# Kernel optimization log

Hardware: AMD Instinct MI355X
Metric: run time of the kernel (lower is better)

## Reference

```python
import jax, jax.numpy as jnp
import numpy as np

B, S, D = 4, 4096, 2048
H, HD = 16, 128
FFN = 8192
CAP = 0.25
TOP_K = int(S * CAP)  # 1024
EPS = 1e-6


def rmsnorm(x, g):
    return x * jax.lax.rsqrt(jnp.mean(x * x, axis=-1, keepdims=True) + EPS) * g


def apply_rope(x, cos, sin):
    # x: [b,t,h,hd]; cos/sin: [t, hd//2]
    half = x.shape[-1] // 2
    x1, x2 = x[..., :half], x[..., half:]
    c = cos[None, :, None, :]
    s = sin[None, :, None, :]
    return jnp.concatenate([x1 * c - x2 * s, x1 * s + x2 * c], axis=-1)


def transformer_block(x, mask, freqs_cis, g1, wq, wk, wv, wo, g2, w1, w3, w2):
    b, t, d = x.shape
    cos, sin = freqs_cis[..., 0], freqs_cis[..., 1]
    h = rmsnorm(x, g1)
    q = (h @ wq).reshape(b, t, H, HD)
    k = (h @ wk).reshape(b, t, H, HD)
    v = (h @ wv).reshape(b, t, H, HD)
    q = apply_rope(q, cos, sin)
    k = apply_rope(k, cos, sin)
    scores = jnp.einsum('bqhd,bkhd->bhqk', q, k) / np.sqrt(HD) + mask[None, None]
    attn = jax.nn.softmax(scores, axis=-1)
    o = jnp.einsum('bhqk,bkhd->bqhd', attn, v).reshape(b, t, d) @ wo
    x = x + o
    h2 = rmsnorm(x, g2)
    x = x + (jax.nn.silu(h2 @ w1) * (h2 @ w3)) @ w2
    return x, None


def setup_inputs() -> dict:
    key = jax.random.key(0)
    ks = jax.random.split(key, 12)
    w = lambda k, shp: jax.random.normal(k, shp, dtype=jnp.float32) * 0.02
    return {
        'x': jax.random.normal(ks[0], (B, S, D), dtype=jnp.float32),
        'mask': jnp.zeros((TOP_K, TOP_K), dtype=jnp.float32),
        'freqs_cis': jax.random.uniform(ks[1], (TOP_K, HD // 2, 2), dtype=jnp.float32),
        'w_router': w(ks[2], (D,)),
        'g1': jnp.ones((D,), dtype=jnp.float32),
        'wq': w(ks[3], (D, D)),
        'wk': w(ks[4], (D, D)),
        'wv': w(ks[5], (D, D)),
        'wo': w(ks[6], (D, D)),
        'g2': jnp.ones((D,), dtype=jnp.float32),
        'w1': w(ks[7], (D, FFN)),
        'w3': w(ks[8], (D, FFN)),
        'w2': w(ks[9], (FFN, D)),
    }


def reference(x, mask, freqs_cis, w_router, g1, wq, wk, wv, wo, g2, w1, w3, w2):
    b, s, d = x.shape
    # router: Linear(dim, 1, bias=False) -> [b, s]
    router_logits = jnp.einsum('bsd,d->bs', x, w_router)
    vals, idx = jax.lax.top_k(router_logits, TOP_K)  # [b, k]
    # sort selected indices ascending; permute weights to match (softmax is
    # permutation-equivariant so softmax-then-permute == torch's gather order)
    order = jnp.argsort(idx, axis=1)
    sel = jnp.take_along_axis(idx, order, axis=1)          # [b, k]
    w_sel = jnp.take_along_axis(vals, order, axis=1)       # [b, k]
    r_weights = jax.nn.softmax(w_sel, axis=1)[..., None]   # [b, k, 1]
    filtered_x = jnp.take_along_axis(x, sel[..., None], axis=1)  # [b, k, d]
    x_out, _ = transformer_block(filtered_x, mask, freqs_cis, g1, wq, wk, wv, wo, g2, w1, w3, w2)
    xw_out = r_weights * x_out
    b_idx = jnp.arange(b)[:, None]
    out = x.at[b_idx, sel].add(xw_out)
    return out
```

## Files before the change

kernel.cpp:

```cpp
#include <hip/hip_runtime.h>
#include <cstdint>
#include <cstddef>

#define NB 4
#define NS 4096
#define ND 2048
#define NH 16
#define NHD 128
#define NT 1024
#define NF 8192

typedef __bf16 bf16;
typedef __bf16 bf16x8 __attribute__((ext_vector_type(8)));
typedef __bf16 bf16x4 __attribute__((ext_vector_type(4)));
typedef float  f32x4  __attribute__((ext_vector_type(4)));

typedef const __attribute__((address_space(1))) void* gptr_t;
typedef __attribute__((address_space(3))) void* lptr_t;

__device__ __forceinline__ float wave_sum(float v) {
#pragma unroll
    for (int off = 32; off > 0; off >>= 1) v += __shfl_xor(v, off);
    return v;
}
__device__ __forceinline__ float wave_max(float v) {
#pragma unroll
    for (int off = 32; off > 0; off >>= 1) v = fmaxf(v, __shfl_xor(v, off));
    return v;
}

__global__ __launch_bounds__(256) void router_k(const float* __restrict__ x,
                                                const float* __restrict__ wr,
                                                float* __restrict__ logits) {
    __shared__ float r4[4];
    long long row = blockIdx.x;
    const float4* xr = (const float4*)(x + row * ND);
    const float4* w4 = (const float4*)wr;
    float p = 0.f;
    for (int i = threadIdx.x; i < ND / 4; i += 256) {
        float4 a = xr[i], b = w4[i];
        p += a.x * b.x + a.y * b.y + a.z * b.z + a.w * b.w;
    }
    p = wave_sum(p);
    if ((threadIdx.x & 63) == 0) r4[threadIdx.x >> 6] = p;
    __syncthreads();
    if (threadIdx.x == 0) logits[row] = r4[0] + r4[1] + r4[2] + r4[3];
}

__global__ __launch_bounds__(1024) void topk_k(const float* __restrict__ logits,
                                               int* __restrict__ sel,
                                               float* __restrict__ rw) {
    __shared__ unsigned long long keys[NS];
    __shared__ float r16[16];
    __shared__ float bmax, bsum;
    const int bb = blockIdx.x;
    const int tid = threadIdx.x;
    const float* lg = logits + (long long)bb * NS;

    for (int i = tid; i < NS; i += 1024) {
        unsigned u = __float_as_uint(lg[i]);
        u = (u & 0x80000000u) ? ~u : (u | 0x80000000u);
        keys[i] = ((unsigned long long)u << 32) | (unsigned)(NS - 1 - i);
    }
    __syncthreads();
    for (int k = 2; k <= NS; k <<= 1) {
        for (int j = k >> 1; j > 0; j >>= 1) {
            for (int i = tid; i < NS; i += 1024) {
                int ixj = i ^ j;
                if (ixj > i) {
                    unsigned long long a = keys[i], c = keys[ixj];
                    bool up = ((i & k) == 0);
                    if (up ? (a < c) : (a > c)) { keys[i] = c; keys[ixj] = a; }
                }
            }
            __syncthreads();
        }
    }
    unsigned long long a0 = keys[tid];
    __syncthreads();
    {
        unsigned idx_ = NS - 1 - (unsigned)(a0 & 0xFFFFFFFFu);
        unsigned uval = (unsigned)(a0 >> 32);
        keys[tid] = ((unsigned long long)idx_ << 32) | uval;
    }
    __syncthreads();
    for (int k = 2; k <= NT; k <<= 1) {
        for (int j = k >> 1; j > 0; j >>= 1) {
            int i = tid, ixj = i ^ j;
            if (i < NT && ixj > i) {
                unsigned long long a = keys[i], c = keys[ixj];
                bool up = ((i & k) == 0);
                if (up ? (a > c) : (a < c)) { keys[i] = c; keys[ixj] = a; }
            }
            __syncthreads();
        }
    }
    unsigned long long kk = keys[tid];
    int si = (int)(kk >> 32);
    unsigned u = (unsigned)(kk & 0xFFFFFFFFu);
    u = (u & 0x80000000u) ? (u ^ 0x80000000u) : ~u;
    float val = __uint_as_float(u);

    const int wid = tid >> 6, lane = tid & 63;
    float mx = wave_max(val);
    if (lane == 0) r16[wid] = mx;
    __syncthreads();
    if (tid == 0) {
        float m = r16[0];
        for (int i = 1; i < 16; i++) m = fmaxf(m, r16[i]);
        bmax = m;
    }
    __syncthreads();
    float e = __expf(val - bmax);
    float s = wave_sum(e);
    if (lane == 0) r16[wid] = s;
    __syncthreads();
    if (tid == 0) {
        float t = 0.f;
        for (int i = 0; i < 16; i++) t += r16[i];
        bsum = t;
    }
    __syncthreads();
    sel[bb * NT + tid] = si;
    rw[bb * NT + tid] = e / bsum;
}

__global__ __launch_bounds__(256) void gather_k(const float* __restrict__ x,
                                                const int* __restrict__ sel,
                                                float* __restrict__ xf) {
    int gid = blockIdx.x * 256 + threadIdx.x;
    int col = gid & (ND / 4 - 1);
    int row = gid >> 9;
    int bb = row >> 10;
    int s = sel[row];
    ((float4*)xf)[gid] = ((const float4*)x)[((long long)bb * NS + s) * (ND / 4) + col];
}

__global__ __launch_bounds__(256) void rmsnorm_k(const float* __restrict__ x,
                                                 const float* __restrict__ g,
                                                 bf16* __restrict__ out) {
    __shared__ float r4[4];
    __shared__ float scl;
    long long row = blockIdx.x;
    const float4* xr = (const float4*)(x + row * ND);
    int i0 = threadIdx.x, i1 = threadIdx.x + 256;
    float4 a = xr[i0], b = xr[i1];
    float ss = a.x * a.x + a.y * a.y + a.z * a.z + a.w * a.w +
               b.x * b.x + b.y * b.y + b.z * b.z + b.w * b.w;
    ss = wave_sum(ss);
    if ((threadIdx.x & 63) == 0) r4[threadIdx.x >> 6] = ss;
    __syncthreads();
    if (threadIdx.x == 0)
        scl = rsqrtf((r4[0] + r4[1] + r4[2] + r4[3]) * (1.0f / ND) + 1e-6f);
    __syncthreads();
    float s = scl;
    const float4* g4 = (const float4*)g;
    float4 ga = g4[i0], gb = g4[i1];
    bf16x4 o0, o1;
    o0[0] = (bf16)(a.x * s * ga.x); o0[1] = (bf16)(a.y * s * ga.y);
    o0[2] = (bf16)(a.z * s * ga.z); o0[3] = (bf16)(a.w * s * ga.w);
    o1[0] = (bf16)(b.x * s * gb.x); o1[1] = (bf16)(b.y * s * gb.y);
    o1[2] = (bf16)(b.z * s * gb.z); o1[3] = (bf16)(b.w * s * gb.w);
    *(bf16x4*)(out + row * ND + i0 * 4) = o0;
    *(bf16x4*)(out + row * ND + i1 * 4) = o1;
}

__global__ __launch_bounds__(256) void transpose_to_bf16(const float* __restrict__ in,
                                                         bf16* __restrict__ out,
                                                         int R, int C) {
    __shared__ float tile[32][33];
    int bx = blockIdx.x * 32;
    int by = blockIdx.y * 32;
    int tx = threadIdx.x & 31;
    int ty = threadIdx.x >> 5;
#pragma unroll
    for (int i = 0; i < 4; i++)
        tile[ty + 8 * i][tx] = in[(long long)(by + ty + 8 * i) * C + bx + tx];
    __syncthreads();
#pragma unroll
    for (int i = 0; i < 4; i++)
        out[(long long)(bx + ty + 8 * i) * R + by + tx] = (bf16)tile[tx][ty + 8 * i];
}

__global__ __launch_bounds__(256) void rope_qk_k(const bf16* __restrict__ QKV,
                                                 const float* __restrict__ fr,
                                                 bf16* __restrict__ Q,
                                                 bf16* __restrict__ K) {
    int gid = blockIdx.x * 256 + threadIdx.x;
    int hd = gid & 63;
    int h = (gid >> 6) & 15;
    int t = (gid >> 10) & (NT - 1);
    int bb = gid >> 20;
    float c = fr[t * 128 + hd * 2 + 0];
    float s = fr[t * 128 + hd * 2 + 1];
    long long base = ((long long)bb * NT + t) * (3 * ND) + h * NHD;
    float q1 = (float)QKV[base + hd],      q2 = (float)QKV[base + hd + 64];
    float k1 = (float)QKV[base + ND + hd], k2 = (float)QKV[base + ND + hd + 64];
    long long ob = (((long long)(bb * NH + h)) * NT + t) * NHD;
    Q[ob + hd]      = (bf16)(q1 * c - q2 * s);
    Q[ob + hd + 64] = (bf16)(q1 * s + q2 * c);
    K[ob + hd]      = (bf16)(k1 * c - k2 * s);
    K[ob + hd + 64] = (bf16)(k1 * s + k2 * c);
}

__global__ __launch_bounds__(256) void vtr_k(const bf16* __restrict__ QKV,
                                             bf16* __restrict__ Vt) {
    __shared__ bf16 tile[64][136];
    const int tt = blockIdx.x * 64;
    const int bh = blockIdx.y;
    const int bb = bh >> 4, h = bh & 15;
    const int tid = threadIdx.x;

    const int lt = tid >> 4;
    const int ld = (tid & 15) * 8;
#pragma unroll
    for (int i = 0; i < 4; i++) {
        int t = i * 16 + lt;
        bf16x8 v = *(const bf16x8*)(QKV + ((size_t)(bb * NT) + tt + t) * (3 * ND)
                                    + 2 * ND + h * NHD + ld);
        *(bf16x8*)&tile[t][ld] = v;
    }
    __syncthreads();

    const int d = tid >> 1;
    const int j0 = (tid & 1) * 32;
    bf16 tmp[32];
#pragma unroll
    for (int j = 0; j < 32; j++) tmp[j] = tile[j0 + j][d];
    bf16* dst = Vt + ((size_t)bh * NHD + d) * NT + tt + j0;
#pragma unroll
    for (int j = 0; j < 4; j++)
        *(bf16x8*)(dst + j * 8) = *(const bf16x8*)(tmp + j * 8);
}

__global__ __launch_bounds__(256) void copy_k(const float4* __restrict__ in,
                                              float4* __restrict__ out, long long n) {
    for (long long i = (long long)blockIdx.x * 256 + threadIdx.x; i < n;
         i += (long long)gridDim.x * 256)
        out[i] = in[i];
}

__global__ __launch_bounds__(256, 2) void flash_k(
    const bf16* __restrict__ Qr,
    const bf16* __restrict__ Kr,
    const bf16* __restrict__ Vt,
    bf16* __restrict__ O) {
    __shared__ char lds[81920];

    const int tid = threadIdx.x;
    const int lane = tid & 63;
    const int w = tid >> 6;
    const int lm = lane & 15, lq = lane >> 4;
    const int lm7 = lm & 7;

    const int bh = blockIdx.y;
    const int q0 = blockIdx.x * 128;
    const bf16* Qb = Qr + (size_t)bh * NT * NHD;
    const bf16* Kb = Kr + (size_t)bh * NT * NHD;
    const bf16* Vb = Vt + (size_t)bh * NHD * NT;

    const int krow = tid >> 4;
    const int kc_s = (tid & 15);
    const int vrow = tid >> 3;
    const int vc_s = (tid & 7);

    bf16x8 q[2][4];
#pragma unroll
    for (int mi = 0; mi < 2; mi++)
#pragma unroll
        for (int ks = 0; ks < 4; ks++)
            q[mi][ks] = *(const bf16x8*)(Qb + (size_t)(q0 + w * 32 + mi * 16 + lm) * NHD
                                         + lq * 8 + ks * 32);

    f32x4 o0[8], o1[8];
#pragma unroll
    for (int i = 0; i < 8; i++) {
        f32x4 zz = {0.f, 0.f, 0.f, 0.f};
        o0[i] = zz; o1[i] = zz;
    }
    float m0[4], m1[4], l0[4], l1[4];
#pragma unroll
    for (int r = 0; r < 4; r++) {
        m0[r] = -3.0e38f; m1[r] = -3.0e38f; l0[r] = 0.f; l1[r] = 0.f;
    }

    char* Pb = lds + 65536 + w * 4096;
    const float kscal = 0.08838834764831845f * 1.4426950408889634f;

#pragma unroll
    for (int i = 0; i < 4; i++) {
        int row = i * 16 + krow;
        __builtin_amdgcn_global_load_lds(
            (gptr_t)(Kb + (size_t)row * NHD + (kc_s ^ (row & 7)) * 8),
            (lptr_t)(lds + i * 4096 + tid * 16), 16, 0, 0);
    }
#pragma unroll
    for (int i = 0; i < 4; i++) {
        int row = i * 32 + vrow;
        __builtin_amdgcn_global_load_lds(
            (gptr_t)(Vb + (size_t)row * NT + (vc_s ^ (row & 7)) * 8),
            (lptr_t)(lds + 32768 + i * 4096 + tid * 16), 16, 0, 0);
    }
    __syncthreads();

    for (int c = 0; c < 16; ++c) {
        char* Kl = lds + (c & 1) * 16384;
        char* Vl = lds + 32768 + (c & 1) * 16384;

        if (c < 15) {
            const int key1 = (c + 1) * 64;
            char* Kd = lds + ((c + 1) & 1) * 16384;
            char* Vd = lds + 32768 + ((c + 1) & 1) * 16384;
#pragma unroll
            for (int i = 0; i < 4; i++) {
                int row = i * 16 + krow;
                __builtin_amdgcn_global_load_lds(
                    (gptr_t)(Kb + (size_t)(key1 + row) * NHD + (kc_s ^ (row & 7)) * 8),
                    (lptr_t)(Kd + i * 4096 + tid * 16), 16, 0, 0);
            }
#pragma unroll
            for (int i = 0; i < 4; i++) {
                int row = i * 32 + vrow;
                __builtin_amdgcn_global_load_lds(
                    (gptr_t)(Vb + (size_t)row * NT + key1 + (vc_s ^ (row & 7)) * 8),
                    (lptr_t)(Vd + i * 4096 + tid * 16), 16, 0, 0);
            }
        }

        f32x4 s0[4], s1[4];
#pragma unroll
        for (int ni = 0; ni < 4; ni++) {
            f32x4 zz = {0.f, 0.f, 0.f, 0.f};
            s0[ni] = zz; s1[ni] = zz;
        }
        __builtin_amdgcn_s_setprio(1);
#pragma unroll
        for (int ni = 0; ni < 4; ni++) {
#pragma unroll
            for (int ks = 0; ks < 4; ks++) {
                bf16x8 kf = *(const bf16x8*)(Kl + (lm + 16 * ni) * 256
                                             + (((lq + 4 * ks) ^ lm7) << 4));
                s0[ni] = __builtin_amdgcn_mfma_f32_16x16x32_bf16(q[0][ks], kf, s0[ni], 0, 0, 0);
                s1[ni] = __builtin_amdgcn_mfma_f32_16x16x32_bf16(q[1][ks], kf, s1[ni], 0, 0, 0);
            }
        }
        __builtin_amdgcn_s_setprio(0);

#pragma unroll
        for (int ni = 0; ni < 4; ni++)
#pragma unroll
            for (int r = 0; r < 4; r++) {
                s0[ni][r] *= kscal;
                s1[ni][r] *= kscal;
            }

        float sc0[4], sc1[4];
#pragma unroll
        for (int r = 0; r < 4; r++) {
            float a0 = fmaxf(fmaxf(s0[0][r], s0[1][r]), fmaxf(s0[2][r], s0[3][r]));
            float a1 = fmaxf(fmaxf(s1[0][r], s1[1][r]), fmaxf(s1[2][r], s1[3][r]));
#pragma unroll
            for (int o = 1; o < 16; o <<= 1) {
                a0 = fmaxf(a0, __shfl_xor(a0, o));
                a1 = fmaxf(a1, __shfl_xor(a1, o));
            }
            float mn0 = fmaxf(m0[r], a0);
            float mn1 = fmaxf(m1[r], a1);
            sc0[r] = exp2f(m0[r] - mn0);
            sc1[r] = exp2f(m1[r] - mn1);
            m0[r] = mn0; m1[r] = mn1;

            float rs0 = 0.f, rs1 = 0.f;
#pragma unroll
            for (int ni = 0; ni < 4; ni++) {
                float p0 = exp2f(s0[ni][r] - mn0);
                float p1 = exp2f(s1[ni][r] - mn1);
                s0[ni][r] = p0; s1[ni][r] = p1;
                rs0 += p0; rs1 += p1;
            }
#pragma unroll
            for (int o = 1; o < 16; o <<= 1) {
                rs0 += __shfl_xor(rs0, o);
                rs1 += __shfl_xor(rs1, o);
            }
            l0[r] = l0[r] * sc0[r] + rs0;
            l1[r] = l1[r] * sc1[r] + rs1;
        }
#pragma unroll
        for (int ni = 0; ni < 8; ni++)
#pragma unroll
            for (int r = 0; r < 4; r++) {
                o0[ni][r] *= sc0[r];
                o1[ni][r] *= sc1[r];
            }

#pragma unroll
        for (int ni = 0; ni < 4; ni++)
#pragma unroll
            for (int r = 0; r < 4; r++) {
                int q_l0 = lq * 4 + r;
                int q_l1 = 16 + q_l0;
                int cw = (lm >> 3) + 2 * ni;
                *(bf16*)(Pb + q_l0 * 128 + ((cw ^ (q_l0 & 7)) << 4) + (lm7 << 1)) =
                    (bf16)s0[ni][r];
                *(bf16*)(Pb + q_l1 * 128 + ((cw ^ (q_l1 & 7)) << 4) + (lm7 << 1)) =
                    (bf16)s1[ni][r];
            }
        asm volatile("s_waitcnt lgkmcnt(0)" ::: "memory");
        __builtin_amdgcn_sched_barrier(0);

        __builtin_amdgcn_s_setprio(1);
#pragma unroll
        for (int ks = 0; ks < 2; ks++) {
            bf16x8 pa0 = *(const bf16x8*)(Pb + lm * 128 + (((lq + 4 * ks) ^ lm7) << 4));
            bf16x8 pa1 = *(const bf16x8*)(Pb + (lm + 16) * 128 + (((lq + 4 * ks) ^ lm7) << 4));
#pragma unroll
            for (int ni = 0; ni < 8; ni++) {
                bf16x8 vf = *(const bf16x8*)(Vl + (lm + 16 * ni) * 128
                                             + (((lq + 4 * ks) ^ lm7) << 4));
                o0[ni] = __builtin_amdgcn_mfma_f32_16x16x32_bf16(pa0, vf, o0[ni], 0, 0, 0);
                o1[ni] = __builtin_amdgcn_mfma_f32_16x16x32_bf16(pa1, vf, o1[ni], 0, 0, 0);
            }
        }
        __builtin_amdgcn_s_setprio(0);

        __syncthreads();
    }

    const int bb = bh >> 4, h = bh & 15;
    float rl0[4], rl1[4];
#pragma unroll
    for (int r = 0; r < 4; r++) { rl0[r] = 1.f / l0[r]; rl1[r] = 1.f / l1[r]; }
#pragma unroll
    for (int ni = 0; ni < 8; ni++) {
#pragma unroll
        for (int r = 0; r < 4; r++) {
            int col = h * 128 + lm + 16 * ni;
            long long r0 = (long long)bb * NT + q0 + w * 32 + lq * 4 + r;
            O[(r0) * ND + col]      = (bf16)(o0[ni][r] * rl0[r]);
            O[(r0 + 16) * ND + col] = (bf16)(o1[ni][r] * rl1[r]);
        }
    }
}

#define G256_SB() __builtin_amdgcn_sched_barrier(0)
#define G256_LGKM(n) do { asm volatile("s_waitcnt lgkmcnt(" #n ")" ::: "memory"); \
    __builtin_amdgcn_sched_barrier(0); } while (0)
#define G256_VMC(n) do { asm volatile("s_waitcnt vmcnt(" #n ")" ::: "memory"); \
    __builtin_amdgcn_sched_barrier(0); } while (0)

#define MFMA_Q(mlo, nlo) do { \
    __builtin_amdgcn_s_setprio(1); \
    _Pragma("unroll") \
    for (int _ks = 0; _ks < 2; _ks++) \
    _Pragma("unroll") \
    for (int _mi = 0; _mi < 4; _mi++) \
    _Pragma("unroll") \
    for (int _ni = 0; _ni < 2; _ni++) \
        acc[(mlo) + _mi][(nlo) + _ni] = __builtin_amdgcn_mfma_f32_16x16x32_bf16( \
            a[(mlo) + _mi][_ks], b[(nlo) + _ni][_ks], acc[(mlo) + _mi][(nlo) + _ni], \
            0, 0, 0); \
    __builtin_amdgcn_s_setprio(0); \
} while (0)

template <int MODE>
__global__ __launch_bounds__(512, 2) void gemm256(
    const bf16* __restrict__ A, int lda,
    const bf16* __restrict__ Bt, int ldb,
    void* __restrict__ Cv, int ldc,
    int K, float alpha,
    const bf16* __restrict__ Bt2,
    const float* __restrict__ res, const int* __restrict__ selp,
    const float* __restrict__ rwp, float* __restrict__ outp) {

    constexpr bool DUALB = (MODE == 6);
    constexpr bool N128  = (MODE == 2 || MODE == 5);
    constexpr bool NI4   = !N128;
    constexpr int  BBUF  = N128 ? 16384 : 32768;
    constexpr int  BUFS  = 32768 + BBUF;
    constexpr int  bw    = (DUALB || N128) ? 32 : 64;
    constexpr int  bStep2 = DUALB ? 16384 : 4096;
    constexpr int  NIE   = (DUALB || N128) ? 2 : 4;
    __shared__ char smem[2 * BUFS];

    const int tid = threadIdx.x;
    const int lane = tid & 63;
    const int wid = tid >> 6;
    const int wm = wid >> 2, wn = wid & 3;
    const int lm = lane & 15, lq = lane >> 4;

    const int nx = gridDim.x;
    const int orig = blockIdx.y * nx + blockIdx.x;
    const int xcd = orig & 7;
    const int r_ = orig >> 3;
    const int mi_ = r_ & 7, ni_ = r_ >> 3;
    const int nT = (DUALB || N128) ? 128 : 256;
    const int m0 = ((xcd >> 2) * 8 + mi_) * 256;
    const int n0 = ((xcd & 3) * (nx >> 2) + ni_) * nT;
    const long long kz = (long long)blockIdx.z * K;

    const int srow = tid >> 3;
    const int skc = ((tid & 7) ^ (srow & 7)) * 8;
    const long long stA = (long long)64 * lda;
    const long long stB = (long long)64 * ldb;
    const bf16* gA = A + (long long)(m0 + srow) * lda + kz + skc;
    const bf16* gB0 = Bt + (long long)(n0 + srow) * ldb + kz + skc;
    const bf16* gB2 = DUALB ? Bt2 + (long long)(n0 + srow) * ldb + kz + skc
                            : gB0 + 2 * stB;

    char* sm = (char*)smem;
    const int sdst = tid * 16;

    auto stage = [&](int c, int t) {
        char* lA = sm + c * BUFS + sdst;
        long long ko = (long long)t * 64;
#pragma unroll
        for (int i = 0; i < 4; i++)
            __builtin_amdgcn_global_load_lds((gptr_t)(gA + i * stA + ko),
                                             (lptr_t)(lA + i * 8192), 16, 0, 0);
        char* lB = sm + c * BUFS + 32768 + sdst;
        __builtin_amdgcn_global_load_lds((gptr_t)(gB0 + ko), (lptr_t)lB, 16, 0, 0);
        __builtin_amdgcn_global_load_lds((gptr_t)(gB0 + stB + ko),
                                         (lptr_t)(lB + 8192), 16, 0, 0);
        if constexpr (NI4) {
            __builtin_amdgcn_global_load_lds((gptr_t)(gB2 + ko),
                                             (lptr_t)(lB + 16384), 16, 0, 0);
            __builtin_amdgcn_global_load_lds((gptr_t)(gB2 + stB + ko),
                                             (lptr_t)(lB + 24576), 16, 0, 0);
        }
    };

    const int aoff = (wm * 128 + lm) * 128 + ((lq ^ (lm & 7)) << 4);
    const int boff = (wn * bw + lm) * 128 + ((lq ^ (lm & 7)) << 4);

    f32x4 acc[8][4];
#pragma unroll
    for (int i = 0; i < 8; i++)
#pragma unroll
        for (int j = 0; j < 4; j++) {
            f32x4 zz = {0.f, 0.f, 0.f, 0.f};
            acc[i][j] = zz;
        }
    bf16x8 a[8][2], b[4][2];

    auto ldA4 = [&](char* bA, int lo) {
#pragma unroll
        for (int mi2 = 0; mi2 < 4; mi2++) {
            a[lo + mi2][0] = *(const bf16x8*)(bA + aoff + (lo + mi2) * 2048);
            a[lo + mi2][1] = *(const bf16x8*)(bA + (aoff ^ 64) + (lo + mi2) * 2048);
        }
    };
    auto ldB2 = [&](char* bB, int lo) {
#pragma unroll
        for (int ni2 = 0; ni2 < 2; ni2++) {
            int ix = lo + ni2;
            int o = boff + (ix & 1) * 2048 + (ix >> 1) * bStep2;
            b[ix][0] = *(const bf16x8*)(bB + o);
            b[ix][1] = *(const bf16x8*)(bB + (o ^ 64));
        }
    };

    const int NTk = K >> 6;

    stage(0, 0);
    stage(1, 1);
    if constexpr (NI4) { G256_VMC(8); } else { G256_VMC(6); }
    __builtin_amdgcn_s_barrier();
    G256_SB();

    for (int t = 0; t < NTk; ++t) {
        const int c = t & 1;
        char* bA = sm + c * BUFS;
        char* bB = bA + 32768;

        ldA4(bA, 0);
        ldB2(bB, 0);
        G256_SB();
        if constexpr (NI4) {
            ldB2(bB, 2);
            G256_SB();
        }
        ldA4(bA, 4);
        G256_SB();

        if constexpr (NI4) { G256_LGKM(12); } else { G256_LGKM(8); }
        MFMA_Q(0, 0);
        if constexpr (NI4) {
            G256_LGKM(8);
            MFMA_Q(0, 2);
        }
        G256_LGKM(0);
        __builtin_amdgcn_s_barrier();
        G256_SB();
        const bool more = (t + 2 < NTk);
        if (more) stage(c, t + 2);
        G256_SB();
        MFMA_Q(4, 0);
        if constexpr (NI4) MFMA_Q(4, 2);
        if (more) {
            if constexpr (NI4) { G256_VMC(8); } else { G256_VMC(6); }
        } else {
            G256_VMC(0);
        }
        __builtin_amdgcn_s_barrier();
        G256_SB();
    }

    if constexpr (MODE == 6) {
        bf16* C = (bf16*)Cv;
#pragma unroll
        for (int mi = 0; mi < 8; mi++) {
#pragma unroll
            for (int ni = 0; ni < 2; ni++) {
                const int row = m0 + wm * 128 + mi * 16 + lq * 4;
                const int col = n0 + wn * 32 + ni * 16 + lm;
#pragma unroll
                for (int r = 0; r < 4; r++) {
                    float v1 = acc[mi][ni][r];
                    float v3 = acc[mi][ni + 2][r];
                    C[(long long)(row + r) * ldc + col] =
                        (bf16)((v1 / (1.f + __expf(-v1))) * v3);
                }
            }
        }
    } else {
#pragma unroll
        for (int mi = 0; mi < 8; mi++) {
#pragma unroll
            for (int ni = 0; ni < NIE; ni++) {
                const int row = m0 + wm * 128 + mi * 16 + lq * 4;
                const int col = n0 + wn * bw + ni * 16 + lm;
#pragma unroll
                for (int r = 0; r < 4; r++) {
                    float v = alpha * acc[mi][ni][r];
                    long long rr = row + r;
                    if constexpr (MODE == 0) {
                        bf16* C = (bf16*)Cv;
                        C[rr * ldc + col] = (bf16)v;
                    } else if constexpr (MODE == 2) {
                        float* C = (float*)Cv;
                        C[rr * ldc + col] += v;
                    } else {
                        int bb2 = (int)(rr >> 10);
                        int s = selp[rr];
                        float add = rwp[rr] * (v + res[rr * (long long)ND + col]);
                        outp[((long long)bb2 * NS + s) * ND + col] += add;
                    }
                }
            }
        }
    }
}

extern "C" void kernel_launch(void* const* d_in, const int* in_sizes, int n_in,
                              void* d_out, int out_size, void* d_ws, size_t ws_size,
                              hipStream_t stream) {
    const float* x  = (const float*)d_in[0];
    const float* fr = (const float*)d_in[2];
    const float* wr = (const float*)d_in[3];
    const float* g1 = (const float*)d_in[4];
    const float* wq = (const float*)d_in[5];
    const float* wk = (const float*)d_in[6];
    const float* wv = (const float*)d_in[7];
    const float* wo = (const float*)d_in[8];
    const float* g2 = (const float*)d_in[9];
    const float* w1 = (const float*)d_in[10];
    const float* w3 = (const float*)d_in[11];
    const float* w2 = (const float*)d_in[12];
    float* out = (float*)d_out;

    char* ws = (char*)d_ws;
    size_t off = 0;
    auto take = [&](size_t bytes) -> char* {
        char* p = ws + off;
        off += (bytes + 255) & ~(size_t)255;
        return p;
    };
    int*   sel    = (int*)take((size_t)NB * NT * 4);
    float* rw     = (float*)take((size_t)NB * NT * 4);
    float* logits = (float*)take((size_t)NB * NS * 4);
    float* xf     = (float*)take((size_t)NB * NT * ND * 4);
    bf16*  hbuf   = (bf16*)take((size_t)NB * NT * ND * 2);
    bf16*  wqkv_t = (bf16*)take((size_t)3 * ND * ND * 2);
    bf16*  wo_t   = (bf16*)take((size_t)ND * ND * 2);
    bf16*  Obuf   = (bf16*)take((size_t)NB * NT * ND * 2);
    char* xr = ws + off;
    bf16* QKV = (bf16*)xr;
    bf16* Qr  = QKV + (size_t)NB * NT * 3 * ND;
    bf16* Kr  = Qr + (size_t)NB * NT * ND;
    bf16* Vt  = Kr + (size_t)NB * NT * ND;
    bf16* w1_t  = (bf16*)xr;
    bf16* w3_t  = w1_t + (size_t)ND * NF;
    bf16* w2_t  = w3_t + (size_t)ND * NF;
    bf16* inter = w2_t + (size_t)ND * NF;

    router_k<<<NB * NS, 256, 0, stream>>>(x, wr, logits);
    topk_k<<<NB, 1024, 0, stream>>>(logits, sel, rw);
    gather_k<<<(NB * NT * ND / 4) / 256, 256, 0, stream>>>(x, sel, xf);
    rmsnorm_k<<<NB * NT, 256, 0, stream>>>(xf, g1, hbuf);

    dim3 tg(ND / 32, ND / 32);
    transpose_to_bf16<<<tg, 256, 0, stream>>>(wq, wqkv_t, ND, ND);
    transpose_to_bf16<<<tg, 256, 0, stream>>>(wk, wqkv_t + (size_t)ND * ND, ND, ND);
    transpose_to_bf16<<<tg, 256, 0, stream>>>(wv, wqkv_t + (size_t)2 * ND * ND, ND, ND);
    transpose_to_bf16<<<tg, 256, 0, stream>>>(wo, wo_t, ND, ND);

    gemm256<0><<<dim3(3 * ND / 256, NB * NT / 256, 1), 512, 0, stream>>>(
        hbuf, ND, wqkv_t, ND, QKV, 3 * ND, ND, 1.0f,
        nullptr, nullptr, nullptr, nullptr, nullptr);

    rope_qk_k<<<(NB * NT * NH * 64) / 256, 256, 0, stream>>>(QKV, fr, Qr, Kr);
    vtr_k<<<dim3(NT / 64, NB * NH), 256, 0, stream>>>(QKV, Vt);

    flash_k<<<dim3(NT / 128, NB * NH), 256, 0, stream>>>(Qr, Kr, Vt, Obuf);

    gemm256<2><<<dim3(ND / 128, NB * NT / 256, 1), 512, 0, stream>>>(
        Obuf, ND, wo_t, ND, xf, ND, ND, 1.0f,
        nullptr, nullptr, nullptr, nullptr, nullptr);

    rmsnorm_k<<<NB * NT, 256, 0, stream>>>(xf, g2, hbuf);

    transpose_to_bf16<<<dim3(NF / 32, ND / 32), 256, 0, stream>>>(w1, w1_t, ND, NF);
    transpose_to_bf16<<<dim3(NF / 32, ND / 32), 256, 0, stream>>>(w3, w3_t, ND, NF);
    transpose_to_bf16<<<dim3(ND / 32, NF / 32), 256, 0, stream>>>(w2, w2_t, NF, ND);

    gemm256<6><<<dim3(NF / 128, NB * NT / 256, 1), 512, 0, stream>>>(
        hbuf, ND, w1_t, ND, inter, NF, ND, 1.0f,
        w3_t, nullptr, nullptr, nullptr, nullptr);

    copy_k<<<8192, 256, 0, stream>>>((const float4*)x, (float4*)out,
                                     (long long)NB * NS * ND / 4);
    gemm256<5><<<dim3(ND / 128, NB * NT / 256, 1), 512, 0, stream>>>(
        inter, NF, w2_t, NF, nullptr, ND, NF, 1.0f,
        nullptr, xf, sel, rw, out);
}
```

Before: 1.236 ms.

## Halve GEMM K-tile to 32 and shrink LDS buffers for occupancy

Cuts the per-stage K depth of the 256-wide GEMM from 64 to 32, which halves the A and B LDS buffers and changes the swizzle, staging loads, fragment loads and wait counts to match. The smaller shared-memory footprint is meant to ease LDS pressure and raise occupancy. In exchange the loop runs twice as many iterations, with more barriers and less MFMA work per synchronisation. It also drops the split-K offset (blockIdx.z), so any caller that relied on it would change behaviour.

Result: slower. 1.370 ms (+10.8%).

```diff
diff --git a/kernel.cpp b/kernel.cpp
--- a/kernel.cpp
+++ b/kernel.cpp
@@ -452,13 +452,11 @@
 #define MFMA_Q(mlo, nlo) do { \
     __builtin_amdgcn_s_setprio(1); \
     _Pragma("unroll") \
-    for (int _ks = 0; _ks < 2; _ks++) \
-    _Pragma("unroll") \
     for (int _mi = 0; _mi < 4; _mi++) \
     _Pragma("unroll") \
     for (int _ni = 0; _ni < 2; _ni++) \
         acc[(mlo) + _mi][(nlo) + _ni] = __builtin_amdgcn_mfma_f32_16x16x32_bf16( \
-            a[(mlo) + _mi][_ks], b[(nlo) + _ni][_ks], acc[(mlo) + _mi][(nlo) + _ni], \
+            a[(mlo) + _mi], b[(nlo) + _ni], acc[(mlo) + _mi][(nlo) + _ni], \
             0, 0, 0); \
     __builtin_amdgcn_s_setprio(0); \
 } while (0)
@@ -476,10 +474,10 @@
     constexpr bool DUALB = (MODE == 6);
     constexpr bool N128  = (MODE == 2 || MODE == 5);
     constexpr bool NI4   = !N128;
-    constexpr int  BBUF  = N128 ? 16384 : 32768;
-    constexpr int  BUFS  = 32768 + BBUF;
+    constexpr int  ABUF  = 16384;
+    constexpr int  BBUF  = N128 ? 8192 : 16384;
+    constexpr int  BUFS  = ABUF + BBUF;
     constexpr int  bw    = (DUALB || N128) ? 32 : 64;
-    constexpr int  bStep2 = DUALB ? 16384 : 4096;
     constexpr int  NIE   = (DUALB || N128) ? 2 : 4;
     __shared__ char smem[2 * BUFS];
 
@@ -497,41 +495,34 @@
     const int nT = (DUALB || N128) ? 128 : 256;
     const int m0 = ((xcd >> 2) * 8 + mi_) * 256;
     const int n0 = ((xcd & 3) * (nx >> 2) + ni_) * nT;
-    const long long kz = (long long)blockIdx.z * K;
-
-    const int srow = tid >> 3;
-    const int skc = ((tid & 7) ^ (srow & 7)) * 8;
-    const long long stA = (long long)64 * lda;
-    const long long stB = (long long)64 * ldb;
-    const bf16* gA = A + (long long)(m0 + srow) * lda + kz + skc;
-    const bf16* gB0 = Bt + (long long)(n0 + srow) * ldb + kz + skc;
-    const bf16* gB2 = DUALB ? Bt2 + (long long)(n0 + srow) * ldb + kz + skc
-                            : gB0 + 2 * stB;
+
+    const int srow = tid >> 2;
+    const int skc = ((tid & 3) ^ ((tid >> 4) & 3)) * 8;
+    const long long stA128 = (long long)128 * lda;
+    const bf16* gA = A + (long long)(m0 + srow) * lda + skc;
+    const bf16* gBa = Bt + (long long)(n0 + srow) * ldb + skc;
+    const bf16* gBb = DUALB ? Bt2 + (long long)(n0 + srow) * ldb + skc
+                            : gBa + (long long)128 * ldb;
 
     char* sm = (char*)smem;
     const int sdst = tid * 16;
 
     auto stage = [&](int c, int t) {
+        long long ko = (long long)t * 32;
         char* lA = sm + c * BUFS + sdst;
-        long long ko = (long long)t * 64;
-#pragma unroll
-        for (int i = 0; i < 4; i++)
-            __builtin_amdgcn_global_load_lds((gptr_t)(gA + i * stA + ko),
-                                             (lptr_t)(lA + i * 8192), 16, 0, 0);
-        char* lB = sm + c * BUFS + 32768 + sdst;
-        __builtin_amdgcn_global_load_lds((gptr_t)(gB0 + ko), (lptr_t)lB, 16, 0, 0);
-        __builtin_amdgcn_global_load_lds((gptr_t)(gB0 + stB + ko),
-                                         (lptr_t)(lB + 8192), 16, 0, 0);
-        if constexpr (NI4) {
-            __builtin_amdgcn_global_load_lds((gptr_t)(gB2 + ko),
-                                             (lptr_t)(lB + 16384), 16, 0, 0);
-            __builtin_amdgcn_global_load_lds((gptr_t)(gB2 + stB + ko),
-                                             (lptr_t)(lB + 24576), 16, 0, 0);
-        }
+        __builtin_amdgcn_global_load_lds((gptr_t)(gA + ko), (lptr_t)lA, 16, 0, 0);
+        __builtin_amdgcn_global_load_lds((gptr_t)(gA + stA128 + ko),
+                                         (lptr_t)(lA + 8192), 16, 0, 0);
+        char* lB = sm + c * BUFS + ABUF + sdst;
+        __builtin_amdgcn_global_load_lds((gptr_t)(gBa + ko), (lptr_t)lB, 16, 0, 0);
+        if constexpr (NI4)
+            __builtin_amdgcn_global_load_lds((gptr_t)(gBb + ko),
+                                             (lptr_t)(lB + 8192), 16, 0, 0);
     };
 
-    const int aoff = (wm * 128 + lm) * 128 + ((lq ^ (lm & 7)) << 4);
-    const int boff = (wn * bw + lm) * 128 + ((lq ^ (lm & 7)) << 4);
+    const int aswz = (lq ^ (lm >> 2)) << 4;
+    const int aoff = (wm * 128 + lm) * 64 + aswz;
+    const int boffL = ((NI4 && !DUALB) ? wn * 64 : wn * 32) * 64 + lm * 64 + aswz;
 
     f32x4 acc[8][4];
 #pragma unroll
@@ -541,37 +532,38 @@
             f32x4 zz = {0.f, 0.f, 0.f, 0.f};
             acc[i][j] = zz;
         }
-    bf16x8 a[8][2], b[4][2];
+    bf16x8 a[8], b[4];
 
     auto ldA4 = [&](char* bA, int lo) {
 #pragma unroll
-        for (int mi2 = 0; mi2 < 4; mi2++) {
-            a[lo + mi2][0] = *(const bf16x8*)(bA + aoff + (lo + mi2) * 2048);
-            a[lo + mi2][1] = *(const bf16x8*)(bA + (aoff ^ 64) + (lo + mi2) * 2048);
-        }
+        for (int mi2 = 0; mi2 < 4; mi2++)
+            a[lo + mi2] = *(const bf16x8*)(bA + aoff + (lo + mi2) * 1024);
     };
     auto ldB2 = [&](char* bB, int lo) {
 #pragma unroll
         for (int ni2 = 0; ni2 < 2; ni2++) {
             int ix = lo + ni2;
-            int o = boff + (ix & 1) * 2048 + (ix >> 1) * bStep2;
-            b[ix][0] = *(const bf16x8*)(bB + o);
-            b[ix][1] = *(const bf16x8*)(bB + (o ^ 64));
+            int o;
+            if constexpr (DUALB)
+                o = (ix >> 1) * 8192 + boffL + (ix & 1) * 1024;
+            else
+                o = boffL + ix * 1024;
+            b[ix] = *(const bf16x8*)(bB + o);
         }
     };
 
-    const int NTk = K >> 6;
+    const int NTk = K >> 5;
 
     stage(0, 0);
     stage(1, 1);
-    if constexpr (NI4) { G256_VMC(8); } else { G256_VMC(6); }
+    if constexpr (NI4) { G256_VMC(4); } else { G256_VMC(3); }
     __builtin_amdgcn_s_barrier();
     G256_SB();
 
     for (int t = 0; t < NTk; ++t) {
         const int c = t & 1;
         char* bA = sm + c * BUFS;
-        char* bB = bA + 32768;
+        char* bB = bA + ABUF;
 
         ldA4(bA, 0);
         ldB2(bB, 0);
@@ -583,10 +575,10 @@
         ldA4(bA, 4);
         G256_SB();
 
-        if constexpr (NI4) { G256_LGKM(12); } else { G256_LGKM(8); }
+        if constexpr (NI4) { G256_LGKM(6); } else { G256_LGKM(4); }
         MFMA_Q(0, 0);
         if constexpr (NI4) {
-            G256_LGKM(8);
+            G256_LGKM(4);
             MFMA_Q(0, 2);
         }
         G256_LGKM(0);
@@ -598,7 +590,7 @@
         MFMA_Q(4, 0);
         if constexpr (NI4) MFMA_Q(4, 2);
         if (more) {
-            if constexpr (NI4) { G256_VMC(8); } else { G256_VMC(6); }
+            if constexpr (NI4) { G256_VMC(4); } else { G256_VMC(3); }
         } else {
             G256_VMC(0);
         }
```
